# Optimization experiments

Measured on AMD Instinct MI355X. Metric: run time of the kernel, lower is better.

The kernel has to match this reference:

```python
import jax, jax.numpy as jnp
import numpy as np

B, S, DIN, H, N, L_S4, L_RES, ED = 512, 500, 14, 128, 256, 4, 6, 256


def setup_inputs() -> dict:
    key = jax.random.key(0)
    ks = jax.random.split(key, 32)
    f = jnp.float32
    rn = lambda k, sh, s: jax.random.normal(k, sh, f) * s
    inp = {
        'x': rn(ks[0], (B, S, DIN), 1.0),
        'timesteps': jax.random.randint(ks[1], (B,), 0, 1000),
        'mask': (jax.random.uniform(ks[2], (B, S, 1)) < 0.9).astype(f),
        'observed': rn(ks[3], (B, S, DIN), 1.0),
        'W_in': rn(ks[4], (DIN, H), DIN ** -0.5), 'b_in': jnp.zeros((H,), f),
        'time_W1': rn(ks[5], (ED, 2 * H), ED ** -0.5), 'time_b1': jnp.zeros((2 * H,), f),
        'time_W2': rn(ks[6], (2 * H, H), (2 * H) ** -0.5), 'time_b2': jnp.zeros((H,), f),
        's4_ln_g': jnp.ones((L_S4, H), f), 's4_ln_b': jnp.zeros((L_S4, H), f),
        's4_logA': jnp.log(0.5 * jnp.ones((L_S4, H, N), f)),
        's4_Aim': jnp.broadcast_to(np.pi * jnp.arange(N, dtype=f), (L_S4, H, N)).copy(),
        's4_Cre': rn(ks[7], (L_S4, H, N), 0.5 ** 0.5),
        's4_Cim': rn(ks[8], (L_S4, H, N), 0.5 ** 0.5),
        's4_D': rn(ks[9], (L_S4, H), 1.0),
        's4_logdt': jax.random.uniform(ks[10], (L_S4, H), f, np.log(0.001), np.log(0.1)),
        's4_Wo': rn(ks[11], (L_S4, H, H), H ** -0.5), 's4_bo': jnp.zeros((L_S4, H), f),
        'res_ln_g': jnp.ones((L_RES, H), f), 'res_ln_b': jnp.zeros((L_RES, H), f),
        'res_W1': rn(ks[12], (L_RES, H, 2 * H), H ** -0.5), 'res_b1': jnp.zeros((L_RES, 2 * H), f),
        'res_W2': rn(ks[13], (L_RES, 2 * H, H), (2 * H) ** -0.5), 'res_b2': jnp.zeros((L_RES, H), f),
        'W_out': rn(ks[14], (H, DIN), H ** -0.5), 'b_out': jnp.zeros((DIN,), f),
    }
    return inp


def _ln(x, g, b):
    m = x.mean(-1, keepdims=True)
    v = ((x - m) ** 2).mean(-1, keepdims=True)
    return (x - m) * jax.lax.rsqrt(v + 1e-5) * g + b


def reference(x, timesteps, mask, observed, W_in, b_in, time_W1, time_b1, time_W2,
              time_b2, s4_ln_g, s4_ln_b, s4_logA, s4_Aim, s4_Cre, s4_Cim, s4_D,
              s4_logdt, s4_Wo, s4_bo, res_ln_g, res_ln_b, res_W1, res_b1, res_W2,
              res_b2, W_out, b_out):
    Bb, Ss, _ = x.shape
    Hh = W_in.shape[1]
    x_cond = x * mask + observed
    # sinusoidal positional encoding gated by mask -> [B,S,H]
    pos = jnp.arange(Ss, dtype=jnp.float32)
    div = jnp.exp(-jnp.log(10000.0) * 2.0 * jnp.arange(Hh // 2, dtype=jnp.float32) / Hh)
    ang = pos[:, None] * div
    pe = jnp.concatenate([jnp.sin(ang), jnp.cos(ang)], -1)  # [S,H]
    h = x_cond @ W_in + b_in + pe[None] * mask
    # S4D layers: prenorm -> FFT causal conv with Vandermonde kernel -> GELU -> proj -> residual
    t_idx = jnp.arange(Ss, dtype=jnp.float32)
    for l in range(s4_logA.shape[0]):
        z = _ln(h, s4_ln_g[l], s4_ln_b[l])
        dt = jnp.exp(s4_logdt[l])[:, None]                       # [H,1]
        A = -jnp.exp(s4_logA[l]) + 1j * s4_Aim[l]                # [H,N]
        dtA = dt * A
        C = (s4_Cre[l] + 1j * s4_Cim[l]) * (jnp.exp(dtA) - 1.0) / A
        V = jnp.exp(dtA[:, :, None] * t_idx)                     # [H,N,S]
        K = 2.0 * jnp.einsum('hn,hnl->hl', C, V).real            # [H,S]
        u = jnp.transpose(z, (0, 2, 1))                          # [B,H,S]
        n = 2 * Ss
        y = jnp.fft.irfft(jnp.fft.rfft(u, n) * jnp.fft.rfft(K, n), n)[..., :Ss]
        y = y + s4_D[l][None, :, None] * u
        y = jax.nn.gelu(jnp.transpose(y, (0, 2, 1)), approximate=False)
        h = h + y @ s4_Wo[l] + s4_bo[l]
    # diffusion time embedding
    half = time_W1.shape[0] // 2
    emb = jnp.log(10000.0) / (half - 1)
    freqs = jnp.exp(-emb * jnp.arange(half, dtype=jnp.float32))
    te = timesteps.astype(jnp.float32)[:, None] * freqs
    te = jnp.concatenate([jnp.sin(te), jnp.cos(te)], -1)
    te = jax.nn.silu(te @ time_W1 + time_b1) @ time_W2 + time_b2
    h = h + te[:, None, :]
    # residual MLP blocks
    for l in range(res_W1.shape[0]):
        z = _ln(h, res_ln_g[l], res_ln_b[l])
        h = h + jax.nn.gelu(z @ res_W1[l] + res_b1[l], approximate=False) @ res_W2[l] + res_b2[l]
    return h @ W_out + b_out
```

## Files before the change

kernel.cpp:

```cpp
#include <hip/hip_runtime.h>
#include <math.h>

#define B_ 512
#define S_ 500
#define SP_ 512
#define DIN_ 14
#define H_ 128
#define N_ 256
#define NT_ 256000

#define SWZ(r) ((((r) ^ ((r) >> 4)) & 15) << 4)

typedef __attribute__((ext_vector_type(8))) short short8v;
typedef __attribute__((ext_vector_type(4))) float f32x4;

__device__ __forceinline__ float gelu_f(float x) {
    float y = 0.7978845608028654f * x * (1.0f + 0.044715f * x * x);
    float t = 1.0f - __fdividef(2.0f, 1.0f + __expf(2.0f * y));
    return 0.5f * x * (1.0f + t);
}
__device__ __forceinline__ short f2bf(float f) {
    unsigned u = __builtin_bit_cast(unsigned, f);
    u += 0x7fffu + ((u >> 16) & 1u);
    return (short)(u >> 16);
}
__device__ __forceinline__ float bf2f(short s) {
    return __builtin_bit_cast(float, ((unsigned)(unsigned short)s) << 16);
}

__global__ __launch_bounds__(256) void k_kmat(
    const float* __restrict__ logA, const float* __restrict__ Aim,
    const float* __restrict__ Cre, const float* __restrict__ Cim,
    const float* __restrict__ logdt, float* __restrict__ Km)
{
    int lh = blockIdx.x;
    __shared__ float  sCr[256], sCi[256], sAr[256];
    __shared__ double sAi[256];
    {
        int n = threadIdx.x;
        int idx = lh * N_ + n;
        double dt  = exp((double)logdt[lh]);
        double Are = -exp((double)logA[idx]);
        double Aiv = (double)Aim[idx];
        double ar  = dt * Are, ai = dt * Aiv;
        double er  = exp(ar);
        double E1r = er * cos(ai) - 1.0, E1i = er * sin(ai);
        double inv = 1.0 / (Are * Are + Aiv * Aiv);
        double qR  = (E1r * Are + E1i * Aiv) * inv;
        double qI  = (E1i * Are - E1r * Aiv) * inv;
        double cre = (double)Cre[idx], cim = (double)Cim[idx];
        sCr[n] = (float)(cre * qR - cim * qI);
        sCi[n] = (float)(cre * qI + cim * qR);
        sAr[n] = (float)ar;
        sAi[n] = ai;
    }
    __syncthreads();
    const double TWO_PI = 6.283185307179586476925286766559;
    const double INV_2PI = 0.15915494309189533576888376337251;
    for (int s = threadIdx.x; s < SP_; s += 256) {
        float acc = 0.0f;
        if (s < S_) {
            float fs = (float)s;
            double fsd = (double)s;
            for (int n = 0; n < N_; ++n) {
                float er = expf(sAr[n] * fs);
                double y = sAi[n] * fsd;
                y -= TWO_PI * rint(y * INV_2PI);
                float sn, cs; sincosf((float)y, &sn, &cs);
                acc += er * (sCr[n] * cs - sCi[n] * sn);
            }
            acc *= 2.0f;
        }
        Km[lh * SP_ + s] = acc;
    }
}

__global__ __launch_bounds__(256) void k_toep(
    const float* __restrict__ Kl, short* __restrict__ Tblk)
{
    int hh = blockIdx.x, d = blockIdx.y;
    const float* Kr = Kl + hh * SP_;
    short* Tb = Tblk + (((size_t)hh * 4 + d) << 14);
    int base = d * 128;
    for (int i = threadIdx.x; i < 16384; i += 256) {
        int s = i >> 7, t = i & 127;
        int diff = base + s - t;
        float v = (diff >= 0 && diff < S_) ? Kr[diff] : 0.f;
        Tb[i] = f2bf(v);
    }
}

__global__ __launch_bounds__(128) void k_petab(float* __restrict__ pet)
{
    int s = blockIdx.x, j = threadIdx.x;
    int jj = j & 63;
    float dv = expf(-0.14391156831212787f * (float)jj);
    float ang = (float)s * dv;
    pet[s * 128 + j] = (j < 64) ? sinf(ang) : cosf(ang);
}

__global__ __launch_bounds__(256) void k_inproj(
    const float* __restrict__ x, const float* __restrict__ mask,
    const float* __restrict__ obs, const float* __restrict__ Win,
    const float* __restrict__ bin, const float* __restrict__ pet,
    float* __restrict__ h, float2* __restrict__ st)
{
    int wid = threadIdx.x >> 6, lane = threadIdx.x & 63;
    int tok0 = blockIdx.x * 16 + wid * 4;
    float w0[DIN_], w1[DIN_];
#pragma unroll
    for (int d = 0; d < DIN_; ++d) {
        w0[d] = Win[d * H_ + lane];
        w1[d] = Win[d * H_ + lane + 64];
    }
    float b0 = bin[lane], b1 = bin[lane + 64];
    for (int t = 0; t < 4; ++t) {
        int tok = tok0 + t;
        int s = tok % S_;
        float m = mask[tok];
        float a0 = b0, a1 = b1;
        const float* xp = x + (size_t)tok * DIN_;
        const float* op = obs + (size_t)tok * DIN_;
#pragma unroll
        for (int d = 0; d < DIN_; ++d) {
            float xc = xp[d] * m + op[d];
            a0 += xc * w0[d];
            a1 += xc * w1[d];
        }
        float h0 = a0 + pet[s * 128 + lane] * m;
        float h1 = a1 + pet[s * 128 + lane + 64] * m;
        float s1 = h0 + h1, s2 = h0 * h0 + h1 * h1;
#pragma unroll
        for (int off = 32; off > 0; off >>= 1) {
            s1 += __shfl_xor(s1, off, 64);
            s2 += __shfl_xor(s2, off, 64);
        }
        float mu = s1 * 0.0078125f;
        float rs = rsqrtf(s2 * 0.0078125f - mu * mu + 1e-5f);
        if (lane == 0) st[tok] = make_float2(mu, rs);
        h[(size_t)tok * H_ + lane] = h0;
        h[(size_t)tok * H_ + lane + 64] = h1;
    }
}

__global__ __launch_bounds__(256) void k_temb(
    const int* __restrict__ ts, const float* __restrict__ W1,
    const float* __restrict__ b1, const float* __restrict__ W2,
    const float* __restrict__ b2, float* __restrict__ te)
{
    __shared__ float feat[256];
    __shared__ float mid[256];
    int b = blockIdx.x, j = threadIdx.x;
    float t = (float)ts[b];
    float fr = expf(-0.07252236513367075f * (float)(j & 127));
    float ang = t * fr;
    feat[j] = (j < 128) ? sinf(ang) : cosf(ang);
    __syncthreads();
    float acc = b1[j];
    for (int k = 0; k < 256; ++k) acc += feat[k] * W1[k * 256 + j];
    mid[j] = acc / (1.0f + expf(-acc));
    __syncthreads();
    if (j < 128) {
        float a2 = b2[j];
        for (int k = 0; k < 256; ++k) a2 += mid[k] * W2[k * 128 + j];
        te[b * 128 + j] = a2;
    }
}

__global__ __launch_bounds__(256) void k_wcast(
    const float* __restrict__ Wo, const float* __restrict__ rW1,
    const float* __restrict__ rW2,
    short* __restrict__ WoT, short* __restrict__ W1T, short* __restrict__ W2T)
{
    int i = blockIdx.x * 256 + threadIdx.x;
    if (i < 65536) {
        int l = i >> 14, r = i & 16383, n = r >> 7, k = r & 127;
        WoT[i] = f2bf(Wo[(size_t)(l * 128 + k) * 128 + n]);
    } else if (i < 262144) {
        int j = i - 65536;
        int l = j >> 15, r = j & 32767, n = r >> 7, k = r & 127;
        W1T[j] = f2bf(rW1[(size_t)(l * 128 + k) * 256 + n]);
    } else if (i < 458752) {
        int j = i - 262144;
        int l = j >> 15, r = j & 32767, n = r >> 8, k = r & 255;
        W2T[j] = f2bf(rW2[(size_t)(l * 256 + k) * 128 + n]);
    }
}

__global__ __launch_bounds__(256) void k_ln_tb(
    const float* __restrict__ h, const float2* __restrict__ stc,
    const float* __restrict__ g, const float* __restrict__ be,
    short* __restrict__ ubt)
{
    int b = blockIdx.x, s0 = blockIdx.y * 64;
    int ntok = min(64, S_ - s0);
    __shared__ float tile[64 * 129];
    __shared__ float mu_[64], rs_[64];
    for (int idx = threadIdx.x; idx < (ntok << 7); idx += 256) {
        int i = idx >> 7, k = idx & 127;
        tile[i * 129 + k] = h[(size_t)(b * S_ + s0 + i) * H_ + k];
    }
    if (threadIdx.x < ntok) {
        float2 ms = stc[(size_t)b * S_ + s0 + threadIdx.x];
        mu_[threadIdx.x] = ms.x; rs_[threadIdx.x] = ms.y;
    }
    __syncthreads();
    for (int idx = threadIdx.x; idx < 128 * 32; idx += 256) {
        int k = idx >> 5, i = (idx & 31) * 2;
        float v0 = (i < ntok)     ? (tile[i * 129 + k]       - mu_[i])     * rs_[i]     * g[k] + be[k] : 0.f;
        float v1 = (i + 1 < ntok) ? (tile[(i + 1) * 129 + k] - mu_[i + 1]) * rs_[i + 1] * g[k] + be[k] : 0.f;
        unsigned lo = (unsigned short)f2bf(v0);
        unsigned hi = (unsigned short)f2bf(v1);
        *(unsigned*)(ubt + ((size_t)b * H_ + k) * SP_ + s0 + i) = lo | (hi << 16);
    }
}

__global__ __launch_bounds__(256) void k_cgemm(
    const short* __restrict__ ubt, const short* __restrict__ Tblk,
    const float* __restrict__ D, short* __restrict__ ybt)
{
    __shared__ short As[16384];
    __shared__ short Bs[16384];
    int hh = blockIdx.x, si = blockIdx.y, bt = blockIdx.z;
    int tid = threadIdx.x;
    int lane = tid & 63, wid = tid >> 6;
    int wm = wid >> 1, wn = wid & 1;
    int fr = lane & 15, ko = (lane >> 4) << 3;
    const short* Ab = ubt + ((size_t)(bt * 128) * H_ + hh) * SP_;

    f32x4 acc[4][4];
    f32x4 zv = {0.f, 0.f, 0.f, 0.f};
#pragma unroll
    for (int m = 0; m < 4; ++m)
#pragma unroll
        for (int n = 0; n < 4; ++n) acc[m][n] = zv;

    for (int tj = 0; tj <= si; ++tj) {
        if (tj) __syncthreads();
        const short* Bb = Tblk + (((size_t)hh * 4 + (si - tj)) << 14);
#pragma unroll
        for (int p = 0; p < 8; ++p) {
            int idx = p * 256 + tid;
            int row = idx >> 4, c16 = idx & 15;
            int byt = row * 256 + ((c16 * 16) ^ SWZ(row));
            *(short8v*)((char*)As + byt) =
                *(const short8v*)(Ab + (size_t)row * (H_ * SP_) + tj * 128 + c16 * 8);
            *(short8v*)((char*)Bs + byt) =
                *(const short8v*)(Bb + row * 128 + c16 * 8);
        }
        __syncthreads();
#pragma unroll
        for (int ks = 0; ks < 4; ++ks) {
            short8v a[4], b[4];
#pragma unroll
            for (int m = 0; m < 4; ++m) {
                int row = wm * 64 + m * 16 + fr;
                int byt = row * 256 + (((ks * 32 + ko) * 2) ^ SWZ(row));
                a[m] = *(const short8v*)((const char*)As + byt);
            }
#pragma unroll
            for (int n = 0; n < 4; ++n) {
                int row = wn * 64 + n * 16 + fr;
                int byt = row * 256 + (((ks * 32 + ko) * 2) ^ SWZ(row));
                b[n] = *(const short8v*)((const char*)Bs + byt);
            }
#pragma unroll
            for (int m = 0; m < 4; ++m)
#pragma unroll
                for (int n = 0; n < 4; ++n)
                    acc[m][n] = __builtin_amdgcn_mfma_f32_16x16x32_bf16(
                        a[m], b[n], acc[m][n], 0, 0, 0);
        }
        if (tj < si) __syncthreads();
    }

    float Dh = D[hh];
#pragma unroll
    for (int m = 0; m < 4; ++m) {
        int b0 = wm * 64 + m * 16 + (lane >> 4) * 4;
#pragma unroll
        for (int n = 0; n < 4; ++n) {
            int sC = si * 128 + wn * 64 + n * 16 + fr;
#pragma unroll
            for (int j = 0; j < 4; ++j) {
                int bg = bt * 128 + b0 + j;
                size_t off = ((size_t)bg * H_ + hh) * SP_ + sC;
                float u = bf2f(ubt[off]);
                ybt[off] = f2bf(gelu_f(acc[m][n][j] + Dh * u));
            }
        }
    }
}

__global__ __launch_bounds__(256) void k_p4(
    const short* __restrict__ ybt, const short* __restrict__ BT,
    const float* __restrict__ bias, const float* __restrict__ te,
    float* __restrict__ hres, float2* __restrict__ st,
    short* __restrict__ un, const float* __restrict__ gn,
    const float* __restrict__ bn)
{
    __shared__ __align__(16) char smem[65536];
    int tid = threadIdx.x;
    int bm = blockIdx.x;
    int bl = bm >> 2, s0t = (bm & 3) * 128;
    int lane = tid & 63, wid = tid >> 6;
    int wm = wid >> 1, wn = wid & 1;
    int fr = lane & 15, ko = (lane >> 4) << 3;

    f32x4 acc[4][4];
    f32x4 zv = {0.f, 0.f, 0.f, 0.f};
#pragma unroll
    for (int m = 0; m < 4; ++m)
#pragma unroll
        for (int n = 0; n < 4; ++n) acc[m][n] = zv;

    const short* Yb = ybt + ((size_t)bl << 16);
#pragma unroll
    for (int p = 0; p < 8; ++p) {
        int idx = p * 256 + tid;
        int hh = idx >> 4, sc = idx & 15;
        short8v y = *(const short8v*)(Yb + (size_t)hh * 512 + s0t + sc * 8);
#pragma unroll
        for (int e = 0; e < 8; ++e) {
            int row = sc * 8 + e;
            int byt = row * 256 + ((hh * 2) ^ SWZ(row));
            *(short*)(smem + byt) = y[e];
        }
    }
#pragma unroll
    for (int p = 0; p < 8; ++p) {
        int idx = p * 256 + tid;
        int row = idx >> 4, c16 = idx & 15;
        int byt = row * 256 + ((c16 * 16) ^ SWZ(row));
        *(short8v*)(smem + 32768 + byt) =
            *(const short8v*)(BT + (size_t)row * 128 + c16 * 8);
    }
    __syncthreads();
#pragma unroll
    for (int ks = 0; ks < 4; ++ks) {
        short8v a[4], b[4];
#pragma unroll
        for (int m = 0; m < 4; ++m) {
            int row = wm * 64 + m * 16 + fr;
            int byt = row * 256 + (((ks * 32 + ko) * 2) ^ SWZ(row));
            a[m] = *(const short8v*)(smem + byt);
        }
#pragma unroll
        for (int n = 0; n < 4; ++n) {
            int row = wn * 64 + n * 16 + fr;
            int byt = row * 256 + (((ks * 32 + ko) * 2) ^ SWZ(row));
            b[n] = *(const short8v*)(smem + 32768 + byt);
        }
#pragma unroll
        for (int m = 0; m < 4; ++m)
#pragma unroll
            for (int n = 0; n < 4; ++n)
                acc[m][n] = __builtin_amdgcn_mfma_f32_16x16x32_bf16(
                    a[m], b[n], acc[m][n], 0, 0, 0);
    }

    float* red = (float*)smem;
    __syncthreads();
#pragma unroll
    for (int m = 0; m < 4; ++m) {
#pragma unroll
        for (int j = 0; j < 4; ++j) {
            int rl = wm * 64 + m * 16 + (lane >> 4) * 4 + j;
            int R = bm * 128 + rl;
            int b_ = R >> 9, s = R & 511;
            bool valid = (s < S_);
            float s1 = 0.f, s2 = 0.f;
#pragma unroll
            for (int n = 0; n < 4; ++n) {
                int C = wn * 64 + n * 16 + fr;
                float v = 0.f;
                if (valid) {
                    float t = te ? te[b_ * 128 + C] : 0.f;
                    size_t go = ((size_t)b_ * S_ + s) * 128 + C;
                    v = hres[go] + acc[m][n][j] + bias[C] + t;
                    hres[go] = v;
                }
                acc[m][n][j] = v;
                s1 += v; s2 += v * v;
            }
            s1 += __shfl_xor(s1, 1, 64); s2 += __shfl_xor(s2, 1, 64);
            s1 += __shfl_xor(s1, 2, 64); s2 += __shfl_xor(s2, 2, 64);
            s1 += __shfl_xor(s1, 4, 64); s2 += __shfl_xor(s2, 4, 64);
            s1 += __shfl_xor(s1, 8, 64); s2 += __shfl_xor(s2, 8, 64);
            if (fr == 0) {
                red[(wn * 128 + rl) * 2]     = s1;
                red[(wn * 128 + rl) * 2 + 1] = s2;
            }
        }
    }
    __syncthreads();
#pragma unroll
    for (int m = 0; m < 4; ++m) {
#pragma unroll
        for (int j = 0; j < 4; ++j) {
            int rl = wm * 64 + m * 16 + (lane >> 4) * 4 + j;
            int R = bm * 128 + rl;
            int b_ = R >> 9, s = R & 511;
            if (s >= S_) continue;
            float s1 = red[rl * 2]     + red[(128 + rl) * 2];
            float s2 = red[rl * 2 + 1] + red[(128 + rl) * 2 + 1];
            float mu = s1 * 0.0078125f;
            float rs = rsqrtf(s2 * 0.0078125f - mu * mu + 1e-5f);
            if (fr == 0 && wn == 0)
                st[(size_t)b_ * S_ + s] = make_float2(mu, rs);
            if (un) {
#pragma unroll
                for (int n = 0; n < 4; ++n) {
                    int C = wn * 64 + n * 16 + fr;
                    un[(((size_t)(b_ * 128 + C)) << 9) + s] =
                        f2bf((acc[m][n][j] - mu) * rs * gn[C] + bn[C]);
                }
            }
        }
    }
}

__global__ __launch_bounds__(512) void k_mlp(
    float* hres, const float2* __restrict__ st,
    const short* __restrict__ W1T, const float* __restrict__ rb1,
    const short* __restrict__ W2T, const float* __restrict__ rb2,
    const float* __restrict__ g6, const float* __restrict__ b6)
{
    __shared__ __align__(16) char As1[32768];
    __shared__ __align__(16) char BsA[32768];
    int tid = threadIdx.x;
    int lane = tid & 63, wid = tid >> 6;
    int wm = wid >> 1, wn = wid & 1;
    int fr = lane & 15, ko = (lane >> 4) << 3;
    int q4 = (lane >> 4) * 4;
    size_t tok0 = (size_t)blockIdx.x * 128;

    f32x4 v[2][4];
#pragma unroll
    for (int m = 0; m < 2; ++m) {
#pragma unroll
        for (int j = 0; j < 4; ++j) {
            int rl = wm * 32 + m * 16 + q4 + j;
            float2 ms = st[tok0 + rl];
            const float* hp = hres + (tok0 + rl) * 128;
#pragma unroll
            for (int n = 0; n < 4; ++n) {
                int C = wn * 64 + n * 16 + fr;
                float hv = hp[C];
                v[m][n][j] = hv;
                float z = (hv - ms.x) * ms.y * g6[C] + b6[C];
                int byt = rl * 256 + ((C * 2) ^ SWZ(rl));
                *(short*)(As1 + byt) = f2bf(z);
            }
        }
    }

    for (int l = 0; l < 6; ++l) {
        const short* W1 = W1T + l * 32768;
        const short* W2 = W2T + l * 32768;
        const float* b1 = rb1 + l * 256;
        const float* b2 = rb2 + l * 128;

        f32x4 acc1[2][8];
        f32x4 zvv = {0.f, 0.f, 0.f, 0.f};
#pragma unroll
        for (int m = 0; m < 2; ++m)
#pragma unroll
            for (int n = 0; n < 8; ++n) acc1[m][n] = zvv;

#pragma unroll
        for (int gy = 0; gy < 2; ++gy) {
#pragma unroll
            for (int p = 0; p < 4; ++p) {
                int idx = p * 512 + tid;
                int row = idx >> 4, c16 = idx & 15;
                int byt = row * 256 + ((c16 * 16) ^ SWZ(row));
                *(short8v*)(BsA + byt) =
                    *(const short8v*)(W1 + (size_t)(gy * 128 + row) * 128 + c16 * 8);
            }
            __syncthreads();
#pragma unroll
            for (int ks = 0; ks < 4; ++ks) {
                short8v a[2], b[4];
#pragma unroll
                for (int m = 0; m < 2; ++m) {
                    int row = wm * 32 + m * 16 + fr;
                    int byt = row * 256 + (((ks * 32 + ko) * 2) ^ SWZ(row));
                    a[m] = *(const short8v*)(As1 + byt);
                }
#pragma unroll
                for (int n = 0; n < 4; ++n) {
                    int row = wn * 64 + n * 16 + fr;
                    int byt = row * 256 + (((ks * 32 + ko) * 2) ^ SWZ(row));
                    b[n] = *(const short8v*)(BsA + byt);
                }
#pragma unroll
                for (int m = 0; m < 2; ++m)
#pragma unroll
                    for (int n = 0; n < 4; ++n)
                        acc1[m][gy * 4 + n] = __builtin_amdgcn_mfma_f32_16x16x32_bf16(
                            a[m], b[n], acc1[m][gy * 4 + n], 0, 0, 0);
            }
            __syncthreads();
        }

        f32x4 acc2[2][4];
#pragma unroll
        for (int m = 0; m < 2; ++m)
#pragma unroll
            for (int n = 0; n < 4; ++n) acc2[m][n] = zvv;
#pragma unroll
        for (int kk = 0; kk < 2; ++kk) {
#pragma unroll
            for (int m = 0; m < 2; ++m) {
#pragma unroll
                for (int j = 0; j < 4; ++j) {
                    int rl = wm * 32 + m * 16 + q4 + j;
#pragma unroll
                    for (int n = 0; n < 4; ++n) {
                        int c = wn * 64 + n * 16 + fr;
                        float y1 = gelu_f(acc1[m][kk * 4 + n][j] + b1[kk * 128 + c]);
                        int byt = rl * 256 + ((c * 2) ^ SWZ(rl));
                        *(short*)(As1 + byt) = f2bf(y1);
                    }
                }
            }
#pragma unroll
            for (int p = 0; p < 4; ++p) {
                int idx = p * 512 + tid;
                int row = idx >> 4, c16 = idx & 15;
                int byt = row * 256 + ((c16 * 16) ^ SWZ(row));
                *(short8v*)(BsA + byt) =
                    *(const short8v*)(W2 + (size_t)row * 256 + kk * 128 + c16 * 8);
            }
            __syncthreads();
#pragma unroll
            for (int ks = 0; ks < 4; ++ks) {
                short8v a[2], b[4];
#pragma unroll
                for (int m = 0; m < 2; ++m) {
                    int row = wm * 32 + m * 16 + fr;
                    int byt = row * 256 + (((ks * 32 + ko) * 2) ^ SWZ(row));
                    a[m] = *(const short8v*)(As1 + byt);
                }
#pragma unroll
                for (int n = 0; n < 4; ++n) {
                    int row = wn * 64 + n * 16 + fr;
                    int byt = row * 256 + (((ks * 32 + ko) * 2) ^ SWZ(row));
                    b[n] = *(const short8v*)(BsA + byt);
                }
#pragma unroll
                for (int m = 0; m < 2; ++m)
#pragma unroll
                    for (int n = 0; n < 4; ++n)
                        acc2[m][n] = __builtin_amdgcn_mfma_f32_16x16x32_bf16(
                            a[m], b[n], acc2[m][n], 0, 0, 0);
            }
            __syncthreads();
        }

#pragma unroll
        for (int m = 0; m < 2; ++m)
#pragma unroll
            for (int n = 0; n < 4; ++n) {
                float bj = b2[wn * 64 + n * 16 + fr];
#pragma unroll
                for (int j = 0; j < 4; ++j)
                    v[m][n][j] += acc2[m][n][j] + bj;
            }
        if (l < 5) {
            float* red = (float*)BsA;
#pragma unroll
            for (int m = 0; m < 2; ++m) {
#pragma unroll
                for (int j = 0; j < 4; ++j) {
                    int rl = wm * 32 + m * 16 + q4 + j;
                    float s1 = 0.f, s2 = 0.f;
#pragma unroll
                    for (int n = 0; n < 4; ++n) {
                        float t = v[m][n][j];
                        s1 += t; s2 += t * t;
                    }
                    s1 += __shfl_xor(s1, 1, 64); s2 += __shfl_xor(s2, 1, 64);
                    s1 += __shfl_xor(s1, 2, 64); s2 += __shfl_xor(s2, 2, 64);
                    s1 += __shfl_xor(s1, 4, 64); s2 += __shfl_xor(s2, 4, 64);
                    s1 += __shfl_xor(s1, 8, 64); s2 += __shfl_xor(s2, 8, 64);
                    if (fr == 0) {
                        red[(wn * 128 + rl) * 2]     = s1;
                        red[(wn * 128 + rl) * 2 + 1] = s2;
                    }
                }
            }
            __syncthreads();
            const float* gl = g6 + (l + 1) * 128;
            const float* bl2 = b6 + (l + 1) * 128;
#pragma unroll
            for (int m = 0; m < 2; ++m) {
#pragma unroll
                for (int j = 0; j < 4; ++j) {
                    int rl = wm * 32 + m * 16 + q4 + j;
                    float s1 = red[rl * 2]     + red[(128 + rl) * 2];
                    float s2 = red[rl * 2 + 1] + red[(128 + rl) * 2 + 1];
                    float mu = s1 * 0.0078125f;
                    float rs = rsqrtf(s2 * 0.0078125f - mu * mu + 1e-5f);
#pragma unroll
                    for (int n = 0; n < 4; ++n) {
                        int C = wn * 64 + n * 16 + fr;
                        float z = (v[m][n][j] - mu) * rs * gl[C] + bl2[C];
                        int byt = rl * 256 + ((C * 2) ^ SWZ(rl));
                        *(short*)(As1 + byt) = f2bf(z);
                    }
                }
            }
            __syncthreads();
        }
    }

#pragma unroll
    for (int m = 0; m < 2; ++m) {
#pragma unroll
        for (int j = 0; j < 4; ++j) {
            int rl = wm * 32 + m * 16 + q4 + j;
            float* hp = hres + (tok0 + rl) * 128;
#pragma unroll
            for (int n = 0; n < 4; ++n)
                hp[wn * 64 + n * 16 + fr] = v[m][n][j];
        }
    }
}

__global__ __launch_bounds__(256) void k_out(
    const float* __restrict__ h, const float* __restrict__ Wout,
    const float* __restrict__ bout, float* __restrict__ out)
{
    __shared__ float wt[16 * 132];
    __shared__ float tile[64 * 132];
    int tok0 = blockIdx.x * 64;
    for (int idx = threadIdx.x; idx < 2048; idx += 256) {
        int j = idx >> 7, k = idx & 127;
        wt[j * 132 + k] = (j < 14) ? Wout[k * 14 + j] : 0.f;
    }
    const float4* hp = (const float4*)(h + (size_t)tok0 * 128);
    for (int idx = threadIdx.x; idx < 2048; idx += 256) {
        int row = idx >> 5, c4 = idx & 31;
        *((float4*)(tile + row * 132) + c4) = hp[idx];
    }
    __syncthreads();
    int i = threadIdx.x >> 2, jq = threadIdx.x & 3;
    float aj[4] = {0.f, 0.f, 0.f, 0.f};
    const float4* tr = (const float4*)(tile + i * 132);
#pragma unroll 8
    for (int kk = 0; kk < 32; ++kk) {
        float4 hv = tr[kk];
#pragma unroll
        for (int r = 0; r < 4; ++r) {
            float4 wv = *((const float4*)(wt + (jq * 4 + r) * 132) + kk);
            aj[r] += hv.x * wv.x + hv.y * wv.y + hv.z * wv.z + hv.w * wv.w;
        }
    }
#pragma unroll
    for (int r = 0; r < 4; ++r) {
        int j = jq * 4 + r;
        if (j < 14)
            out[(size_t)(tok0 + i) * 14 + j] = aj[r] + bout[j];
    }
}

extern "C" void kernel_launch(void* const* d_in, const int* in_sizes, int n_in,
                              void* d_out, int out_size, void* d_ws, size_t ws_size,
                              hipStream_t stream)
{
    (void)in_sizes; (void)n_in; (void)out_size;
    const float* x      = (const float*)d_in[0];
    const int*   tsteps = (const int*)  d_in[1];
    const float* mask   = (const float*)d_in[2];
    const float* obs    = (const float*)d_in[3];
    const float* Win    = (const float*)d_in[4];
    const float* bin    = (const float*)d_in[5];
    const float* tW1    = (const float*)d_in[6];
    const float* tb1    = (const float*)d_in[7];
    const float* tW2    = (const float*)d_in[8];
    const float* tb2    = (const float*)d_in[9];
    const float* lng4   = (const float*)d_in[10];
    const float* lnb4   = (const float*)d_in[11];
    const float* logA   = (const float*)d_in[12];
    const float* Aim    = (const float*)d_in[13];
    const float* Cre    = (const float*)d_in[14];
    const float* Cim    = (const float*)d_in[15];
    const float* Dp     = (const float*)d_in[16];
    const float* logdt  = (const float*)d_in[17];
    const float* Wo     = (const float*)d_in[18];
    const float* bo     = (const float*)d_in[19];
    const float* lng6   = (const float*)d_in[20];
    const float* lnb6   = (const float*)d_in[21];
    const float* rW1    = (const float*)d_in[22];
    const float* rb1    = (const float*)d_in[23];
    const float* rW2    = (const float*)d_in[24];
    const float* rb2    = (const float*)d_in[25];
    const float* Woutp  = (const float*)d_in[26];
    const float* boutp  = (const float*)d_in[27];

    float*  ws  = (float*)d_ws;
    float*  h   = ws;
    float*  Km  = h + 32768000;
    float*  te  = Km + 262144;
    float2* st  = (float2*)(te + 65536);
    float*  pet = (float*)st + 512000;
    short*  WoT = (short*)(pet + 64000);
    short*  W1T = WoT + 65536;
    short*  W2T = W1T + 196608;
    float*  big = (float*)(W2T + 196608);
    size_t  wf  = ws_size / sizeof(float);
    size_t  fixed = 33901056;
    size_t  avail = (wf > fixed) ? (wf - fixed) : 0;

    bool flowA = (avail >= 29360128);

    k_kmat<<<512, 256, 0, stream>>>(logA, Aim, Cre, Cim, logdt, Km);
    k_petab<<<S_, 128, 0, stream>>>(pet);
    k_inproj<<<NT_ / 16, 256, 0, stream>>>(x, mask, obs, Win, bin, pet, h, st);
    k_temb<<<B_, 256, 0, stream>>>(tsteps, tW1, tb1, tW2, tb2, te);
    k_wcast<<<1792, 256, 0, stream>>>(Wo, rW1, rW2, WoT, W1T, W2T);

    if (flowA) {
        short* ubtA = (short*)big;
        short* ubtB = ubtA + 16777216;
        short* ybt  = ubtB + 16777216;
        short* Tblk = ybt + 16777216;

        k_ln_tb<<<dim3(256, 8), 256, 0, stream>>>(h, st, lng4, lnb4, ubtA);
        k_ln_tb<<<dim3(256, 8), 256, 0, stream>>>(
            h + (size_t)256 * S_ * H_, st + (size_t)256 * S_, lng4, lnb4, ubtB);

        for (int l = 0; l < 4; ++l) {
            k_toep<<<dim3(H_, 4), 256, 0, stream>>>(Km + (size_t)l * H_ * SP_, Tblk);
            for (int cb = 0; cb < 2; ++cb) {
                size_t bOff = (size_t)cb * 256;
                float* hb = h + bOff * S_ * H_;
                short* ub = cb ? ubtB : ubtA;
                const float* tep = (l == 3) ? (te + bOff * H_) : (const float*)0;
                short* un = (l < 3) ? ub : (short*)0;
                k_cgemm<<<dim3(H_, 4, 2), 256, 0, stream>>>(ub, Tblk, Dp + l * H_, ybt);
                k_p4<<<1024, 256, 0, stream>>>(
                    ybt, WoT + l * 16384, bo + l * H_, tep, hb, st + bOff * S_,
                    un, lng4 + (l + 1) * H_, lnb4 + (l + 1) * H_);
            }
        }
    } else {
        int CHB = 64;
        for (int c = 256; c >= 64; c >>= 1)
            if ((size_t)c * 65536 + 4194304 <= avail) { CHB = c; break; }
        short* ubt  = (short*)big;
        short* ybt  = ubt + (size_t)CHB * 65536;
        short* Tblk = ybt + (size_t)CHB * 65536;
        int nCB = B_ / CHB;
        for (int l = 0; l < 4; ++l) {
            k_toep<<<dim3(H_, 4), 256, 0, stream>>>(Km + (size_t)l * H_ * SP_, Tblk);
            for (int cb = 0; cb < nCB; ++cb) {
                size_t bOff = (size_t)cb * CHB;
                float* hb = h + bOff * S_ * H_;
                const float* tep = (l == 3) ? (te + bOff * H_) : (const float*)0;
                k_ln_tb<<<dim3(CHB, 8), 256, 0, stream>>>(
                    hb, st + bOff * S_, lng4 + l * H_, lnb4 + l * H_, ubt);
                k_cgemm<<<dim3(H_, 4, CHB / 128), 256, 0, stream>>>(
                    ubt, Tblk, Dp + l * H_, ybt);
                k_p4<<<CHB * 4, 256, 0, stream>>>(
                    ybt, WoT + l * 16384, bo + l * H_, tep, hb, st + bOff * S_,
                    (short*)0, lng4, lnb4);
            }
        }
    }

    k_mlp<<<NT_ / 128, 512, 0, stream>>>(h, st, W1T, rb1, W2T, rb2, lng6, lnb6);

    k_out<<<NT_ / 64, 256, 0, stream>>>(h, Woutp, boutp, (float*)d_out);
}
```

Before: 2.275 ms.

## Use fast float math in kernel-matrix build and stage transposed LN output via LDS

The S4 kernel generation loop switches from double-precision phase reduction and precise expf/sincosf to float arithmetic with a host-side-style fmod pre-reduction and fast intrinsics, cutting FP64 and libm cost. The epilogue that writes the normalized, transposed bf16 activations now stages them in swizzled shared memory and emits 16-byte vectorized global stores instead of scattered 2-byte stores. Padding rows are written as zeros. The float phase computation risks accuracy loss for large s*Aim products.

```diff
diff --git a/kernel.cpp b/kernel.cpp
--- a/kernel.cpp
+++ b/kernel.cpp
@@ -34,8 +34,7 @@
     const float* __restrict__ logdt, float* __restrict__ Km)
 {
     int lh = blockIdx.x;
-    __shared__ float  sCr[256], sCi[256], sAr[256];
-    __shared__ double sAi[256];
+    __shared__ float sCr[256], sCi[256], sAr[256], sAif[256];
     {
         int n = threadIdx.x;
         int idx = lh * N_ + n;
@@ -52,22 +51,20 @@
         sCr[n] = (float)(cre * qR - cim * qI);
         sCi[n] = (float)(cre * qI + cim * qR);
         sAr[n] = (float)ar;
-        sAi[n] = ai;
+        sAif[n] = (float)fmod(ai, 6.283185307179586476925286766559);
     }
     __syncthreads();
-    const double TWO_PI = 6.283185307179586476925286766559;
-    const double INV_2PI = 0.15915494309189533576888376337251;
     for (int s = threadIdx.x; s < SP_; s += 256) {
         float acc = 0.0f;
         if (s < S_) {
             float fs = (float)s;
-            double fsd = (double)s;
             for (int n = 0; n < N_; ++n) {
-                float er = expf(sAr[n] * fs);
-                double y = sAi[n] * fsd;
-                y -= TWO_PI * rint(y * INV_2PI);
-                float sn, cs; sincosf((float)y, &sn, &cs);
-                acc += er * (sCr[n] * cs - sCi[n] * sn);
+                float er = __expf(sAr[n] * fs);
+                float y = sAif[n] * fs;
+                y -= 6.28318530717958648f * rintf(y * 0.159154943091895336f);
+                float sn, cs; __sincosf(y, &sn, &cs);
+                acc = fmaf(er * sCr[n], cs, acc);
+                acc = fmaf(-er * sCi[n], sn, acc);
             }
             acc *= 2.0f;
         }
@@ -360,6 +357,7 @@
     }
 
     float* red = (float*)smem;
+    short* znT = (short*)(smem + 32768);
     __syncthreads();
 #pragma unroll
     for (int m = 0; m < 4; ++m) {
@@ -401,21 +399,31 @@
             int rl = wm * 64 + m * 16 + (lane >> 4) * 4 + j;
             int R = bm * 128 + rl;
             int b_ = R >> 9, s = R & 511;
-            if (s >= S_) continue;
+            bool valid = (s < S_);
             float s1 = red[rl * 2]     + red[(128 + rl) * 2];
             float s2 = red[rl * 2 + 1] + red[(128 + rl) * 2 + 1];
             float mu = s1 * 0.0078125f;
             float rs = rsqrtf(s2 * 0.0078125f - mu * mu + 1e-5f);
-            if (fr == 0 && wn == 0)
+            if (valid && fr == 0 && wn == 0)
                 st[(size_t)b_ * S_ + s] = make_float2(mu, rs);
             if (un) {
 #pragma unroll
                 for (int n = 0; n < 4; ++n) {
                     int C = wn * 64 + n * 16 + fr;
-                    un[(((size_t)(b_ * 128 + C)) << 9) + s] =
-                        f2bf((acc[m][n][j] - mu) * rs * gn[C] + bn[C]);
-                }
-            }
+                    float z = valid ? (acc[m][n][j] - mu) * rs * gn[C] + bn[C] : 0.f;
+                    *(short*)((char*)znT + C * 256 + ((rl * 2) ^ SWZ(C))) = f2bf(z);
+                }
+            }
+        }
+    }
+    if (un) {
+        __syncthreads();
+#pragma unroll
+        for (int p = 0; p < 8; ++p) {
+            int idx = p * 256 + tid;
+            int C = idx >> 4, rlg = idx & 15;
+            short8v z8 = *(const short8v*)((const char*)znT + C * 256 + ((rlg * 16) ^ SWZ(C)));
+            *(short8v*)(un + (((size_t)(bl * 128 + C)) << 9) + s0t + rlg * 8) = z8;
         }
     }
 }
```

New measurement: 2.078 ms. 8.7% less time.
